# Kernel optimization log

Measured on AMD Instinct MI355X. Metric: run time of the kernel, lower is better.

Reference implementation:

```python
import jax, jax.numpy as jnp
import numpy as np

RAY_DIR = jnp.array([0.4395064455, 0.617598629942, 0.652231566745], dtype=jnp.float32)
TOL = 1e-7
CONTACT_THRESH = 25.0   # opt.contact_thresh
COLLISION_THRESH = 25.0  # opt.collision_thresh
BIG = 1e10


def mesh_contains(points, triangles, tri_valid):
    """Moller-Trumbore ray casting (fixed ray dir), parity test.
    points [B,P,3], triangles [B,T,3,3], tri_valid [B,T] -> exterior [B,P] bool."""
    v0, v1, v2 = triangles[:, :, 0, :], triangles[:, :, 1, :], triangles[:, :, 2, :]
    e1 = v1 - v0
    e2 = v2 - v0
    pvec = jnp.cross(jnp.broadcast_to(RAY_DIR, e2.shape), e2)          # [B,T,3]
    dets = jnp.sum(e1 * pvec, -1)                                      # [B,T]
    parallel = jnp.abs(dets) < TOL
    invdet = 1.0 / (dets + 0.1 * TOL)
    tvec = points[:, None, :, :] - v0[:, :, None, :]                   # [B,T,P,3]
    u = jnp.sum(tvec * pvec[:, :, None, :], -1) * invdet[:, :, None]   # [B,T,P]
    qvec = jnp.cross(tvec, e1[:, :, None, :])                          # [B,T,P,3]
    v = jnp.sum(qvec * RAY_DIR, -1) * invdet[:, :, None]
    t = jnp.sum(e2[:, :, None, :] * qvec, -1) * invdet[:, :, None]
    inter = (u > 0) & (u < 1) & (v > 0) & (u + v < 1) & (t > TOL)
    inter = inter & (~parallel & tri_valid)[:, :, None]
    n_hits = jnp.sum(inter.astype(jnp.int32), axis=1)                  # [B,P]
    return (n_hits % 2) == 0


def masked_mean_loss(vals, mask):
    m = mask.astype(vals.dtype)
    tot = m.sum()
    loss = jnp.where(tot > 0, (m * vals).sum() / jnp.maximum(tot, 1.0), 0.0)
    row = m.sum(1)
    losses = jnp.where(row > 0, (m * vals).sum(1) / jnp.maximum(row, 1.0), 0.0)
    return loss, losses


def setup_inputs() -> dict:
    key = jax.random.key(0)
    ks = jax.random.split(key, 6)
    B, Nh, Fh, No, Fo = 8, 778, 1538, 2000, 4000
    hand_verts = jax.random.normal(ks[0], (B, Nh, 3), dtype=jnp.float32)
    hand_faces = jax.random.randint(ks[1], (B, Fh, 3), 0, Nh, dtype=jnp.int32)
    obj_verts = jax.random.normal(ks[2], (B, No, 3), dtype=jnp.float32)
    obj_faces = jax.random.randint(ks[3], (B, Fo, 3), 0, 1200, dtype=jnp.int32)
    obj_vert_splits = 1200 + jax.random.randint(ks[4], (B,), 0, No - 1200 + 1, dtype=jnp.int32)
    obj_face_splits = 2400 + jax.random.randint(ks[5], (B,), 0, Fo - 2400 + 1, dtype=jnp.int32)
    return {"hand_verts": hand_verts, "hand_faces": hand_faces,
            "obj_verts": obj_verts, "obj_faces": obj_faces,
            "obj_vert_splits": obj_vert_splits, "obj_face_splits": obj_face_splits}


def reference(hand_verts, hand_faces, obj_verts, obj_faces, obj_vert_splits, obj_face_splits):
    B, Nh, _ = hand_verts.shape
    No = obj_verts.shape[1]
    Fo = obj_faces.shape[1]
    sg = jax.lax.stop_gradient

    # gather triangles (batched)
    hand_tri = jax.vmap(lambda v, f: v[f])(hand_verts, hand_faces)     # [B,Fh,3,3]
    obj_tri = jax.vmap(lambda v, f: v[f])(obj_verts, obj_faces)        # [B,Fo,3,3]

    face_valid = jnp.arange(Fo)[None, :] < obj_face_splits[:, None]    # [B,Fo]
    vert_valid = jnp.arange(No)[None, :] < obj_vert_splits[:, None]    # [B,No]

    # containment tests run on detached geometry (as in original)
    hand_tri_valid = jnp.ones(hand_tri.shape[:2], dtype=bool)
    exterior_obj = mesh_contains(sg(obj_verts), sg(hand_tri), hand_tri_valid)   # [B,No]
    exterior_hand = mesh_contains(sg(hand_verts), sg(obj_tri), face_valid)      # [B,Nh]

    penetr_o_mask = (~exterior_obj) & vert_valid
    penetr_h_mask = ~exterior_hand

    # ragged squared pairwise distances (bmm form of original), padded cols -> BIG
    rx = jnp.sum(hand_verts * hand_verts, -1)                          # [B,Nh]
    ry = jnp.sum(obj_verts * obj_verts, -1)                            # [B,No]
    zz = jnp.einsum('bnd,bmd->bnm', hand_verts, obj_verts)             # [B,Nh,No]
    dists = rx[:, :, None] + ry[:, None, :] - 2.0 * zz
    dists = jnp.where(vert_valid[:, None, :], dists, BIG)

    minoh_idxs = jnp.argmin(dists, axis=1)                             # [B,No]
    minho_idxs = jnp.argmin(dists, axis=2)                             # [B,Nh]

    results_close = jnp.take_along_axis(obj_verts, minho_idxs[:, :, None], axis=1)    # [B,Nh,3]
    results_o_close = jnp.take_along_axis(hand_verts, minoh_idxs[:, :, None], axis=1)  # [B,No,3]

    # contact_target == 'all'
    anchor_dists = jnp.sqrt(jnp.sum((results_close - hand_verts) ** 2, -1))    # [B,Nh]
    anchor_o_dist = jnp.sqrt(jnp.sum((results_o_close - obj_verts) ** 2, -1))  # [B,No]

    # contact_mode == 'dist_tanh' -> below_dist all ones
    contact_vals = CONTACT_THRESH * jnp.tanh(anchor_dists / CONTACT_THRESH)
    # collision_mode == 'dist_tanh'
    collision_vals = COLLISION_THRESH * jnp.tanh(anchor_dists / COLLISION_THRESH)
    collision_o_vals = COLLISION_THRESH * jnp.tanh(anchor_o_dist / COLLISION_THRESH)
    collision_o_vals = jnp.where(vert_valid, collision_o_vals, 0.0)

    # contact_zones == 'all'
    missed_mask = exterior_hand

    missed_loss, missed_losses = masked_mean_loss(contact_vals, missed_mask)
    penetr_h_loss, penetr_h_losses = masked_mean_loss(collision_vals, penetr_h_mask)
    penetr_o_loss, penetr_o_losses = masked_mean_loss(collision_o_vals, penetr_o_mask)
    penetr_loss = penetr_h_loss + penetr_o_loss
    penetr_losses = penetr_h_losses + penetr_o_losses

    return missed_loss, penetr_loss, missed_losses, penetr_losses
```

## Files before the change

### kernel.cpp

```cpp
#include <hip/hip_runtime.h>


#define RX 0.4395064455f
#define RY 0.617598629942f
#define RZ 0.652231566745f

#define MAXCHUNK_F4 256
#define PTS_PER_BLK 512

struct Params {
    const float* hand_verts; const int* hand_faces;
    const float* obj_verts;  const int* obj_faces;
    const int* ovsplit; const int* ofsplit;
    int* hitsA;
    int* hitsB;
    float* anchor_h; float* anchor_o;
    float* partials;
    unsigned int* done;
    float* out;
    int B, Nh, Fh, No, Fo;
    int pbA, CA, chunkA, blocksA;
    int pbB, CB, chunkB, blocksB;
};

__device__ __forceinline__ void tri_pre_one(const float* __restrict__ vb,
                                            const int* __restrict__ f,
                                            float4* o) {
#pragma clang fp contract(off)
    int i0 = f[0], i1 = f[1], i2 = f[2];
    float v0x = vb[i0*3+0], v0y = vb[i0*3+1], v0z = vb[i0*3+2];
    float v1x = vb[i1*3+0], v1y = vb[i1*3+1], v1z = vb[i1*3+2];
    float v2x = vb[i2*3+0], v2y = vb[i2*3+1], v2z = vb[i2*3+2];
    float e1x = v1x - v0x, e1y = v1y - v0y, e1z = v1z - v0z;
    float e2x = v2x - v0x, e2y = v2y - v0y, e2z = v2z - v0z;
    float px = RY*e2z - RZ*e2y;
    float py = RZ*e2x - RX*e2z;
    float pz = RX*e2y - RY*e2x;
    float det = (e1x*px + e1y*py) + e1z*pz;
    float invdet = 1.0f / (det + 1e-8f);
    if (fabsf(det) < 1e-7f) invdet = 0.0f;
    o[0] = make_float4(v0x, v0y, v0z, invdet);
    o[1] = make_float4(e1x, e1y, e1z, 0.0f);
    o[2] = make_float4(e2x, e2y, e2z, 0.0f);
    o[3] = make_float4(px,  py,  pz,  0.0f);
}

__device__ __forceinline__ int mt_test(float qx, float qy, float qz,
                                       const float4& f0, const float4& f1,
                                       const float4& f2, const float4& f3) {
#pragma clang fp contract(off)
    float tvx = qx - f0.x, tvy = qy - f0.y, tvz = qz - f0.z;
    float u  = ((tvx*f3.x + tvy*f3.y) + tvz*f3.z) * f0.w;
    float qvx = tvy*f1.z - tvz*f1.y;
    float qvy = tvz*f1.x - tvx*f1.z;
    float qvz = tvx*f1.y - tvy*f1.x;
    float v  = ((qvx*RX + qvy*RY) + qvz*RZ) * f0.w;
    float tt = ((f2.x*qvx + f2.y*qvy) + f2.z*qvz) * f0.w;
    bool hit = (u > 0.0f) && (u < 1.0f) && (v > 0.0f) &&
               ((u + v) < 1.0f) && (tt > 1e-7f);
    return hit ? 1 : 0;
}

__device__ __forceinline__ void raycast_vb(const Params& p, int vbid, int tid,
                                           float4* s_tri) {
#pragma clang fp contract(off)
    const float* pts; const float* tverts; const int* tfaces; int* slots;
    int P, T, Nv, c, pb, b, chunk, tlim, plim;
    if (vbid < p.blocksA) {
        int per_b = p.pbA * p.CA;
        b  = vbid / per_b;
        int r = vbid - b * per_b;
        c  = r / p.pbA;
        pb = r - c * p.pbA;
        pts = p.obj_verts; tverts = p.hand_verts; tfaces = p.hand_faces;
        slots = p.hitsA;
        P = p.No; T = p.Fh; Nv = p.Nh; chunk = p.chunkA;
        tlim = p.Fh; plim = min(p.No, p.ovsplit[b]);
    } else {
        int j = vbid - p.blocksA;
        int per_b = p.pbB * p.CB;
        b  = j / per_b;
        int r = j - b * per_b;
        c  = r / p.pbB;
        pb = r - c * p.pbB;
        pts = p.hand_verts; tverts = p.obj_verts; tfaces = p.obj_faces;
        slots = p.hitsB;
        P = p.Nh; T = p.Fo; Nv = p.No; chunk = p.chunkB;
        tlim = min(p.Fo, p.ofsplit[b]); plim = p.Nh;
    }

    int tStart = c * chunk;
    if (tStart >= tlim) return;
    if (pb * PTS_PER_BLK >= plim) return;
    int nTri = min(tStart + chunk, tlim) - tStart;

    if (tid < nTri) {
        int t = tStart + tid;
        tri_pre_one(tverts + (size_t)b * Nv * 3,
                    tfaces + ((size_t)b * T + t) * 3,
                    s_tri + (size_t)tid * 4);
    }

    int p1 = pb * PTS_PER_BLK + tid;
    int p2 = p1 + 256;
    bool act1 = p1 < plim, act2 = p2 < plim;
    float q1x = 0.f, q1y = 0.f, q1z = 0.f;
    float q2x = 0.f, q2y = 0.f, q2z = 0.f;
    if (act1) {
        const float* q = pts + ((size_t)b * P + p1) * 3;
        q1x = q[0]; q1y = q[1]; q1z = q[2];
    }
    if (act2) {
        const float* q = pts + ((size_t)b * P + p2) * 3;
        q2x = q[0]; q2y = q[1]; q2z = q[2];
    }
    __syncthreads();

    if (!act1) return;
    int cnt1 = 0, cnt2 = 0;
    if (__any(act2)) {
        for (int i = 0; i < nTri; ++i) {
            const float4 f0 = s_tri[(i<<2)+0];
            const float4 f1 = s_tri[(i<<2)+1];
            const float4 f2 = s_tri[(i<<2)+2];
            const float4 f3 = s_tri[(i<<2)+3];
            cnt1 += mt_test(q1x, q1y, q1z, f0, f1, f2, f3);
            cnt2 += mt_test(q2x, q2y, q2z, f0, f1, f2, f3);
        }
    } else {
        for (int i = 0; i < nTri; ++i) {
            const float4 f0 = s_tri[(i<<2)+0];
            const float4 f1 = s_tri[(i<<2)+1];
            const float4 f2 = s_tri[(i<<2)+2];
            const float4 f3 = s_tri[(i<<2)+3];
            cnt1 += mt_test(q1x, q1y, q1z, f0, f1, f2, f3);
        }
    }
    int* base = slots + (size_t)b * P;
    if (cnt1)         atomicAdd(&base[p1], cnt1);
    if (act2 && cnt2) atomicAdd(&base[p2], cnt2);
}

__device__ __forceinline__ void min_one(const Params& p, int w, int lane) {
#pragma clang fp contract(off)
    int nHand = p.B * p.Nh;
    const float* refv; const float* loopv; int loopN; float* outp;
    if (w < nHand) {
        int b = w / p.Nh;
        int n = w - b * p.Nh;
        refv  = p.hand_verts + ((size_t)b * p.Nh + n) * 3;
        loopv = p.obj_verts + (size_t)b * p.No * 3;
        loopN = p.ovsplit[b];
        outp  = p.anchor_h + (size_t)b * p.Nh + n;
    } else {
        int j = w - nHand;
        int b = j / p.No;
        int m = j - b * p.No;
        if (m >= p.ovsplit[b]) return;
        refv  = p.obj_verts + ((size_t)b * p.No + m) * 3;
        loopv = p.hand_verts + (size_t)b * p.Nh * 3;
        loopN = p.Nh;
        outp  = p.anchor_o + (size_t)b * p.No + m;
    }
    float hx = refv[0], hy = refv[1], hz = refv[2];
    float rx = (hx*hx + hy*hy) + hz*hz;
    unsigned long long best = ~0ull;
    for (int m = lane; m < loopN; m += 64) {
        float ox = loopv[m*3+0], oy = loopv[m*3+1], oz = loopv[m*3+2];
        float ry = (ox*ox + oy*oy) + oz*oz;
        float zz = (hx*ox + hy*oy) + hz*oz;
        float d = (rx + ry) - 2.0f * zz;
        unsigned long long e = ((unsigned long long)__float_as_uint(d) << 32) | (unsigned)m;
        if (e < best) best = e;
    }
    for (int off = 32; off > 0; off >>= 1) {
        unsigned long long o = __shfl_xor(best, off, 64);
        if (o < best) best = o;
    }
    if (lane == 0) {
        int idx = (best == ~0ull) ? 0 : (int)(best & 0xffffffffu);
        const float* cv = loopv + (size_t)idx * 3;
        float dx = cv[0] - hx, dy = cv[1] - hy, dz = cv[2] - hz;
        *outp = sqrtf((dx*dx + dy*dy) + dz*dz);
    }
}

__global__ __launch_bounds__(256) void mega(Params p) {
    __shared__ float4 s_tri[MAXCHUNK_F4];
    const int tid = threadIdx.x;
    const int bid = blockIdx.x;
    if (bid == 0 && tid == 0) *p.done = 0u;
    const int nRay = p.blocksA + p.blocksB;
    if (bid < nRay) {
        raycast_vb(p, bid, tid, s_tri);
    } else {
        int w = (bid - nRay) * 4 + (tid >> 6);
        if (w < p.B * (p.Nh + p.No)) min_one(p, w, tid & 63);
    }
}

__global__ __launch_bounds__(64) void reduce_fin(Params p) {
    const int r    = blockIdx.x;
    const int b    = r >> 4;
    const int wv   = r & 15;
    const int lane = threadIdx.x;
    const int vt   = wv * 64 + lane;
    float s0=0.f,s1=0.f,s2=0.f,s3=0.f,s4=0.f,s5=0.f;

    for (int n = vt; n < p.Nh; n += 1024) {
        int par = p.hitsB[(size_t)b * p.Nh + n];
        bool ext = (par & 1) == 0;
        float val = 25.0f * tanhf(p.anchor_h[(size_t)b*p.Nh + n] / 25.0f);
        if (ext) { s0 += val; s1 += 1.0f; } else { s2 += val; s3 += 1.0f; }
    }
    int split = p.ovsplit[b];
    for (int m = vt; m < split; m += 1024) {
        int par = p.hitsA[(size_t)b * p.No + m];
        if (par & 1) {
            s4 += 25.0f * tanhf(p.anchor_o[(size_t)b*p.No + m] / 25.0f);
            s5 += 1.0f;
        }
    }
    for (int off = 32; off > 0; off >>= 1) {
        s0 += __shfl_xor(s0, off, 64);
        s1 += __shfl_xor(s1, off, 64);
        s2 += __shfl_xor(s2, off, 64);
        s3 += __shfl_xor(s3, off, 64);
        s4 += __shfl_xor(s4, off, 64);
        s5 += __shfl_xor(s5, off, 64);
    }

    __shared__ bool s_last;
    if (lane == 0) {
        float* q = p.partials + ((size_t)(b * 16 + wv)) * 6;
        q[0]=s0; q[1]=s1; q[2]=s2; q[3]=s3; q[4]=s4; q[5]=s5;
        __threadfence();
        unsigned int old = atomicAdd(p.done, 1u);
        s_last = (old == (unsigned int)(gridDim.x - 1));
    }
    __syncthreads();
    if (!s_last) return;
    __threadfence();

    __shared__ float s_red[16][6];
    if (lane < p.B && lane < 16) {
        int bb = lane;
        float t0=0.f,t1=0.f,t2=0.f,t3=0.f,t4=0.f,t5=0.f;
        for (int w2 = 0; w2 < 16; ++w2) {
            const float* q = p.partials + ((size_t)(bb * 16 + w2)) * 6;
            t0 += q[0]; t1 += q[1]; t2 += q[2];
            t3 += q[3]; t4 += q[4]; t5 += q[5];
        }
        p.out[2 + bb]  = (t1 > 0.f) ? t0 / fmaxf(t1, 1.f) : 0.f;
        float ph       = (t3 > 0.f) ? t2 / fmaxf(t3, 1.f) : 0.f;
        float po       = (t5 > 0.f) ? t4 / fmaxf(t5, 1.f) : 0.f;
        p.out[10 + bb] = ph + po;
        s_red[bb][0]=t0; s_red[bb][1]=t1; s_red[bb][2]=t2;
        s_red[bb][3]=t3; s_red[bb][4]=t4; s_red[bb][5]=t5;
    }
    __syncthreads();
    if (lane == 0) {
        float sm=0.f,cm=0.f,sph=0.f,cph=0.f,spo=0.f,cpo=0.f;
        for (int bb = 0; bb < p.B; ++bb) {
            sm  += s_red[bb][0]; cm  += s_red[bb][1]; sph += s_red[bb][2];
            cph += s_red[bb][3]; spo += s_red[bb][4]; cpo += s_red[bb][5];
        }
        float missed = (cm  > 0.f) ? sm  / fmaxf(cm , 1.f) : 0.f;
        float ph     = (cph > 0.f) ? sph / fmaxf(cph, 1.f) : 0.f;
        float po     = (cpo > 0.f) ? spo / fmaxf(cpo, 1.f) : 0.f;
        p.out[0] = missed;
        p.out[1] = ph + po;
    }
}

extern "C" void kernel_launch(void* const* d_in, const int* in_sizes, int n_in,
                              void* d_out, int out_size, void* d_ws, size_t ws_size,
                              hipStream_t stream) {
    Params p;
    p.hand_verts = (const float*)d_in[0];
    p.hand_faces = (const int*)d_in[1];
    p.obj_verts  = (const float*)d_in[2];
    p.obj_faces  = (const int*)d_in[3];
    p.ovsplit    = (const int*)d_in[4];
    p.ofsplit    = (const int*)d_in[5];
    p.out        = (float*)d_out;

    p.B  = in_sizes[4];
    p.Nh = in_sizes[0] / (3 * p.B);
    p.Fh = in_sizes[1] / (3 * p.B);
    p.No = in_sizes[2] / (3 * p.B);
    p.Fo = in_sizes[3] / (3 * p.B);

    p.CA = 32; p.CB = 64;
    p.chunkA = (p.Fh + p.CA - 1) / p.CA;
    p.chunkB = (p.Fo + p.CB - 1) / p.CB;
    p.pbA = (p.No + PTS_PER_BLK - 1) / PTS_PER_BLK;
    p.pbB = (p.Nh + PTS_PER_BLK - 1) / PTS_PER_BLK;
    p.blocksA = p.pbA * p.CA * p.B;
    p.blocksB = p.pbB * p.CB * p.B;

    char* ws = (char*)d_ws;
    size_t off = 0;
    auto alloc = [&](size_t bytes) -> void* {
        void* q = ws + off;
        off = (off + bytes + 255) & ~(size_t)255;
        return q;
    };
    size_t hitsOff = off;
    p.hitsA    = (int*)   alloc((size_t)p.B * p.No * sizeof(int));
    p.hitsB    = (int*)   alloc((size_t)p.B * p.Nh * sizeof(int));
    size_t hitsBytes = off - hitsOff;
    p.anchor_h = (float*) alloc((size_t)p.B * p.Nh * sizeof(float));
    p.anchor_o = (float*) alloc((size_t)p.B * p.No * sizeof(float));
    p.partials = (float*) alloc((size_t)p.B * 16 * 6 * sizeof(float));
    p.done     = (unsigned int*)alloc(sizeof(unsigned int));

    int totalMin   = p.B * (p.Nh + p.No);
    int nMinBlocks = (totalMin + 3) / 4;
    int grid = p.blocksA + p.blocksB + nMinBlocks;

    hipMemsetAsync((void*)p.hitsA, 0, hitsBytes, stream);
    mega<<<grid, 256, 0, stream>>>(p);
    reduce_fin<<<p.B * 16, 64, 0, stream>>>(p);
}
```

Before: 123.5 us.

## Precompute triangle records in a prep kernel and read them from global memory

Adds a prep kernel that computes each triangle's Moller-Trumbore record once into workspace and also zeroes the hit counters, taking the place of the memset. When the workspace is large enough, the raycast blocks read those records straight from global memory (uniform loads that should hit cache) rather than rebuilding them into shared memory behind a __syncthreads. This removes the gather and precompute that was repeated in every point block, along with the block barrier, but adds a kernel launch and makes the inner loop's loads go through global memory and cache instead of LDS.

```diff
diff --git a/kernel.cpp b/kernel.cpp
--- a/kernel.cpp
+++ b/kernel.cpp
@@ -12,6 +12,8 @@
     const float* hand_verts; const int* hand_faces;
     const float* obj_verts;  const int* obj_faces;
     const int* ovsplit; const int* ofsplit;
+    float4* trecA;
+    float4* trecB;
     int* hitsA;
     int* hitsB;
     float* anchor_h; float* anchor_o;
@@ -21,6 +23,7 @@
     int B, Nh, Fh, No, Fo;
     int pbA, CA, chunkA, blocksA;
     int pbB, CB, chunkB, blocksB;
+    int useG;
 };
 
 __device__ __forceinline__ void tri_pre_one(const float* __restrict__ vb,
@@ -61,10 +64,31 @@
     return hit ? 1 : 0;
 }
 
+__global__ __launch_bounds__(256) void prep(Params p) {
+    int j = blockIdx.x * 256 + threadIdx.x;
+    int nTriA = p.B * p.Fh;
+    int nTriB = p.B * p.Fo;
+    if (j < nTriA) {
+        int b = j / p.Fh, t = j - b * p.Fh;
+        tri_pre_one(p.hand_verts + (size_t)b * p.Nh * 3,
+                    p.hand_faces + ((size_t)b * p.Fh + t) * 3,
+                    p.trecA + (size_t)j * 4);
+    } else if (j < nTriA + nTriB) {
+        int k = j - nTriA;
+        int b = k / p.Fo, t = k - b * p.Fo;
+        tri_pre_one(p.obj_verts + (size_t)b * p.No * 3,
+                    p.obj_faces + ((size_t)b * p.Fo + t) * 3,
+                    p.trecB + (size_t)k * 4);
+    }
+    if (j < p.B * p.No) p.hitsA[j] = 0;
+    if (j < p.B * p.Nh) p.hitsB[j] = 0;
+}
+
 __device__ __forceinline__ void raycast_vb(const Params& p, int vbid, int tid,
                                            float4* s_tri) {
 #pragma clang fp contract(off)
     const float* pts; const float* tverts; const int* tfaces; int* slots;
+    const float4* trec;
     int P, T, Nv, c, pb, b, chunk, tlim, plim;
     if (vbid < p.blocksA) {
         int per_b = p.pbA * p.CA;
@@ -73,7 +97,7 @@
         c  = r / p.pbA;
         pb = r - c * p.pbA;
         pts = p.obj_verts; tverts = p.hand_verts; tfaces = p.hand_faces;
-        slots = p.hitsA;
+        slots = p.hitsA; trec = p.trecA + (size_t)b * p.Fh * 4;
         P = p.No; T = p.Fh; Nv = p.Nh; chunk = p.chunkA;
         tlim = p.Fh; plim = min(p.No, p.ovsplit[b]);
     } else {
@@ -84,7 +108,7 @@
         c  = r / p.pbB;
         pb = r - c * p.pbB;
         pts = p.hand_verts; tverts = p.obj_verts; tfaces = p.obj_faces;
-        slots = p.hitsB;
+        slots = p.hitsB; trec = p.trecB + (size_t)b * p.Fo * 4;
         P = p.Nh; T = p.Fo; Nv = p.No; chunk = p.chunkB;
         tlim = min(p.Fo, p.ofsplit[b]); plim = p.Nh;
     }
@@ -92,13 +116,16 @@
     int tStart = c * chunk;
     if (tStart >= tlim) return;
     if (pb * PTS_PER_BLK >= plim) return;
-    int nTri = min(tStart + chunk, tlim) - tStart;
-
-    if (tid < nTri) {
-        int t = tStart + tid;
-        tri_pre_one(tverts + (size_t)b * Nv * 3,
-                    tfaces + ((size_t)b * T + t) * 3,
-                    s_tri + (size_t)tid * 4);
+    int tEnd = min(tStart + chunk, tlim);
+
+    if (!p.useG) {
+        int nTri = tEnd - tStart;
+        if (tid < nTri) {
+            int t = tStart + tid;
+            tri_pre_one(tverts + (size_t)b * Nv * 3,
+                        tfaces + ((size_t)b * T + t) * 3,
+                        s_tri + (size_t)tid * 4);
+        }
     }
 
     int p1 = pb * PTS_PER_BLK + tid;
@@ -114,26 +141,51 @@
         const float* q = pts + ((size_t)b * P + p2) * 3;
         q2x = q[0]; q2y = q[1]; q2z = q[2];
     }
-    __syncthreads();
-
-    if (!act1) return;
+
     int cnt1 = 0, cnt2 = 0;
-    if (__any(act2)) {
-        for (int i = 0; i < nTri; ++i) {
-            const float4 f0 = s_tri[(i<<2)+0];
-            const float4 f1 = s_tri[(i<<2)+1];
-            const float4 f2 = s_tri[(i<<2)+2];
-            const float4 f3 = s_tri[(i<<2)+3];
-            cnt1 += mt_test(q1x, q1y, q1z, f0, f1, f2, f3);
-            cnt2 += mt_test(q2x, q2y, q2z, f0, f1, f2, f3);
-        }
-    } else {
-        for (int i = 0; i < nTri; ++i) {
-            const float4 f0 = s_tri[(i<<2)+0];
-            const float4 f1 = s_tri[(i<<2)+1];
-            const float4 f2 = s_tri[(i<<2)+2];
-            const float4 f3 = s_tri[(i<<2)+3];
-            cnt1 += mt_test(q1x, q1y, q1z, f0, f1, f2, f3);
+    if (p.useG) {
+        if (!act1) return;
+        const float4* __restrict__ tr = trec + (size_t)tStart * 4;
+        int n = tEnd - tStart;
+        if (__any(act2)) {
+            for (int i = 0; i < n; ++i) {
+                const float4 f0 = tr[(i<<2)+0];
+                const float4 f1 = tr[(i<<2)+1];
+                const float4 f2 = tr[(i<<2)+2];
+                const float4 f3 = tr[(i<<2)+3];
+                cnt1 += mt_test(q1x, q1y, q1z, f0, f1, f2, f3);
+                cnt2 += mt_test(q2x, q2y, q2z, f0, f1, f2, f3);
+            }
+        } else {
+            for (int i = 0; i < n; ++i) {
+                const float4 f0 = tr[(i<<2)+0];
+                const float4 f1 = tr[(i<<2)+1];
+                const float4 f2 = tr[(i<<2)+2];
+                const float4 f3 = tr[(i<<2)+3];
+                cnt1 += mt_test(q1x, q1y, q1z, f0, f1, f2, f3);
+            }
+        }
+    } else {
+        __syncthreads();
+        if (!act1) return;
+        int n = tEnd - tStart;
+        if (__any(act2)) {
+            for (int i = 0; i < n; ++i) {
+                const float4 f0 = s_tri[(i<<2)+0];
+                const float4 f1 = s_tri[(i<<2)+1];
+                const float4 f2 = s_tri[(i<<2)+2];
+                const float4 f3 = s_tri[(i<<2)+3];
+                cnt1 += mt_test(q1x, q1y, q1z, f0, f1, f2, f3);
+                cnt2 += mt_test(q2x, q2y, q2z, f0, f1, f2, f3);
+            }
+        } else {
+            for (int i = 0; i < n; ++i) {
+                const float4 f0 = s_tri[(i<<2)+0];
+                const float4 f1 = s_tri[(i<<2)+1];
+                const float4 f2 = s_tri[(i<<2)+2];
+                const float4 f3 = s_tri[(i<<2)+3];
+                cnt1 += mt_test(q1x, q1y, q1z, f0, f1, f2, f3);
+            }
         }
     }
     int* base = slots + (size_t)b * P;
@@ -299,6 +351,12 @@
     p.blocksA = p.pbA * p.CA * p.B;
     p.blocksB = p.pbB * p.CB * p.B;
 
+    size_t needG = ((size_t)p.B * (p.Fh + p.Fo) * 4 * sizeof(float4)) +
+                   ((size_t)p.B * (p.No + p.Nh) * sizeof(int)) +
+                   ((size_t)p.B * (p.Nh + p.No) * sizeof(float)) +
+                   ((size_t)p.B * 16 * 6 * sizeof(float)) + 4096;
+    p.useG = (ws_size >= needG) ? 1 : 0;
+
     char* ws = (char*)d_ws;
     size_t off = 0;
     auto alloc = [&](size_t bytes) -> void* {
@@ -306,6 +364,12 @@
         off = (off + bytes + 255) & ~(size_t)255;
         return q;
     };
+    if (p.useG) {
+        p.trecA = (float4*)alloc((size_t)p.B * p.Fh * 4 * sizeof(float4));
+        p.trecB = (float4*)alloc((size_t)p.B * p.Fo * 4 * sizeof(float4));
+    } else {
+        p.trecA = nullptr; p.trecB = nullptr;
+    }
     size_t hitsOff = off;
     p.hitsA    = (int*)   alloc((size_t)p.B * p.No * sizeof(int));
     p.hitsB    = (int*)   alloc((size_t)p.B * p.Nh * sizeof(int));
@@ -319,7 +383,12 @@
     int nMinBlocks = (totalMin + 3) / 4;
     int grid = p.blocksA + p.blocksB + nMinBlocks;
 
-    hipMemsetAsync((void*)p.hitsA, 0, hitsBytes, stream);
+    if (p.useG) {
+        int nPrep = (p.B * (p.Fh + p.Fo) + 255) / 256;
+        prep<<<nPrep, 256, 0, stream>>>(p);
+    } else {
+        hipMemsetAsync((void*)p.hitsA, 0, hitsBytes, stream);
+    }
     mega<<<grid, 256, 0, stream>>>(p);
     reduce_fin<<<p.B * 16, 64, 0, stream>>>(p);
 }
```

After: 140.9 us. 1.14x slower.
